# Performance work log

Measured on AMD Instinct MI355X. Metric: run time of the kernel, lower is better.

The kernel has to match this reference:

```python
import jax, jax.numpy as jnp
import numpy as np

H, W, C = 64, 64, 64
B = 64
N_HEADS = 4
CONV_FILTERS = 64
BASIS_DIM = 16


def get_spatial_basis(h, w, d):
    half_d = d // 2
    basis = np.zeros((h, w, d), dtype=np.float32)
    div = np.exp(np.arange(0, half_d, 2, dtype=np.float32) * -np.log(100.0) / half_d)
    h_grid = np.expand_dims(np.arange(0, h, dtype=np.float32), 1)
    w_grid = np.expand_dims(np.arange(0, w, dtype=np.float32), 1)
    basis[:, :, 0:half_d:2] = np.sin(h_grid * div)[:, np.newaxis, :]
    basis[:, :, 1:half_d:2] = np.cos(h_grid * div)[:, np.newaxis, :]
    basis[:, :, half_d::2] = np.sin(w_grid * div)[np.newaxis, :, :]
    basis[:, :, half_d + 1::2] = np.cos(w_grid * div)[np.newaxis, :, :]
    return basis


def setup_inputs() -> dict:
    key = jax.random.key(0)
    ks = jax.random.split(key, 8)
    feat_in = C + BASIS_DIM  # 80 input channels for 1x1 convs
    return {
        "image": jax.random.normal(ks[0], (B, H, W, C), jnp.float32),
        "state1": jax.random.normal(ks[1], (B, 512), jnp.float32),
        "state2": jax.random.normal(ks[2], (B, 512), jnp.float32),
        "extra": jax.random.normal(ks[3], (B, 256), jnp.float32),
        "Wq": jax.random.normal(ks[4], (1024, CONV_FILTERS), jnp.float32) * 0.03,
        "bq": jnp.zeros((CONV_FILTERS,), jnp.float32),
        "Wk": jax.random.normal(ks[5], (feat_in, CONV_FILTERS), jnp.float32) * 0.1,
        "bk": jnp.zeros((CONV_FILTERS,), jnp.float32),
        "Wv": jax.random.normal(ks[6], (feat_in, CONV_FILTERS), jnp.float32) * 0.1,
        "bv": jnp.zeros((CONV_FILTERS,), jnp.float32),
        "spatial_basis": jnp.asarray(get_spatial_basis(H, W, BASIS_DIM)),
    }


def reference(image, state1, state2, extra, Wq, bq, Wk, bk, Wv, bv, spatial_basis):
    b, h, w, _ = image.shape
    nh = N_HEADS
    cf = Wq.shape[1]
    dph = cf // nh  # depth per head

    # concat image with tiled spatial basis -> [B,h,w,C+basis_dim]
    sb = jnp.broadcast_to(spatial_basis[None], (b,) + spatial_basis.shape)
    feats = jnp.concatenate([image, sb], axis=-1)

    # combiner over network-state tensors, then Dense query
    state = jnp.concatenate([state1, state2], axis=-1)  # [B,1024]
    q = state @ Wq + bq                                 # [B,cf]

    # 1x1 convs == per-pixel dense projections
    keys = feats @ Wk + bk    # [B,h,w,cf]
    vals = feats @ Wv + bv    # [B,h,w,cf]

    qh = q.reshape(b, nh, dph)
    kh = keys.reshape(b, h * w, nh, dph)
    vh = vals.reshape(b, h * w, nh, dph)

    # per-head dot scores over spatial positions, softmax over positions
    scores = jnp.einsum('bnd,bpnd->bpn', qh, kh)        # [B,hw,nh]
    attn = jax.nn.softmax(scores, axis=1)
    mean_attn = attn.mean(axis=-1).reshape(b, h, w)

    # weighted sum of values over spatial positions -> [B,cf]
    pooled = jnp.einsum('bpn,bpnd->bnd', attn, vh).reshape(b, cf)

    out = jnp.concatenate([pooled, extra], axis=-1)
    return out, mean_attn
```

## Files before the change

### kernel.cpp

```cpp
#include <hip/hip_runtime.h>
#include <hip/hip_bf16.h>

#define BATCH 64
#define HW    4096
#define PT    128
#define NS    32
#define FR_ST 104
#define FT_ST 136

typedef unsigned int u32;
typedef unsigned short u16;
typedef __attribute__((ext_vector_type(8))) short bf16x8;
typedef __attribute__((ext_vector_type(4))) float f32x4;

__device__ __forceinline__ float bf2f(u16 h) { return __uint_as_float(((u32)h) << 16); }
__device__ __forceinline__ u32 f2bf(float x) {
  u32 b = __float_as_uint(x);
  return (b + 0x7fffu + ((b >> 16) & 1u)) >> 16;
}
__device__ __forceinline__ u32 pkbf(float lo, float hi) { return f2bf(lo) | (f2bf(hi) << 16); }

template<bool F32>
__device__ __forceinline__ float ld(const void* p, size_t i) {
  if (F32) return ((const float*)p)[i];
  return bf2f(((const u16*)p)[i]);
}
template<bool F32>
__device__ __forceinline__ float4 ld4(const void* p, size_t i4) {
  if (F32) return ((const float4*)p)[i4];
  uint2 u = ((const uint2*)p)[i4];
  return make_float4(bf2f(u.x & 0xffff), bf2f(u.x >> 16), bf2f(u.y & 0xffff), bf2f(u.y >> 16));
}
template<bool F32>
__device__ __forceinline__ void st(void* p, size_t i, float v) {
  if (F32) ((float*)p)[i] = v;
  else     ((__hip_bfloat16*)p)[i] = __float2bfloat16(v);
}

__device__ __forceinline__ bool detect_f32(const u16* __restrict__ image) {
  u16 h = image[(threadIdx.x & 63) * 2];
  u32 e = (h >> 7) & 0xFFu;
  unsigned long long m = __ballot(e >= 0x86u);
  return __popcll(m) >= 8;
}

template<bool F32>
__device__ void k1a_body(const void* state1, const void* state2, const void* Wq,
                         float* q_part, float* WslT, float* stt) {
  const int kb = blockIdx.x;
  const int tid = threadIdx.x;
#pragma unroll
  for (int i = 0; i < 4; ++i) {
    const int fidx = i * 256 + tid;
    const int r = fidx >> 4, c4 = fidx & 15;
    float4 v = ld4<F32>(Wq, (size_t)(kb * 64 + r) * 16 + c4);
    WslT[(c4 * 4 + 0) * 68 + r] = v.x;
    WslT[(c4 * 4 + 1) * 68 + r] = v.y;
    WslT[(c4 * 4 + 2) * 68 + r] = v.z;
    WslT[(c4 * 4 + 3) * 68 + r] = v.w;
  }
  const void* src = (kb < 8) ? state1 : state2;
  const int k0q = (kb & 7) * 16;
#pragma unroll
  for (int i = 0; i < 4; ++i) {
    const int fidx = i * 256 + tid;
    const int bb = fidx >> 4, i4 = fidx & 15;
    float4 v = ld4<F32>(src, (size_t)bb * 128 + k0q + i4);
    *(float4*)&stt[bb * 64 + i4 * 4] = v;
  }
  __syncthreads();
  const int j = tid & 63, bg = tid >> 6;
  float acc[16];
#pragma unroll
  for (int b2 = 0; b2 < 16; ++b2) acc[b2] = 0.f;
#pragma unroll
  for (int i4 = 0; i4 < 16; ++i4) {
    float4 wv = *(const float4*)&WslT[j * 68 + i4 * 4];
#pragma unroll
    for (int b2 = 0; b2 < 16; ++b2) {
      float4 sv = *(const float4*)&stt[(bg * 16 + b2) * 64 + i4 * 4];
      acc[b2] += wv.x * sv.x + wv.y * sv.y + wv.z * sv.z + wv.w * sv.w;
    }
  }
#pragma unroll
  for (int b2 = 0; b2 < 16; ++b2)
    q_part[kb * 4096 + (bg * 16 + b2) * 64 + j] = acc[b2];
}

__global__ __launch_bounds__(256) void k1a(
    const void* image, const void* state1, const void* state2, const void* Wq, float* q_part) {
  __shared__ float WslT[64 * 68];
  __shared__ float stt[64 * 64];
  if (detect_f32((const u16*)image)) k1a_body<true >(state1, state2, Wq, q_part, WslT, stt);
  else                               k1a_body<false>(state1, state2, Wq, q_part, WslT, stt);
}

template<bool F32>
__device__ void k1b_body(const float* q_part, const void* bq, const void* Wk, const void* bk,
                         u16* weffbt, float* cb, float* q) {
  const int b = blockIdx.x, tid = threadIdx.x;
  u32* wz = (u32*)(weffbt + (size_t)b * 1664);
  for (int i = tid; i < 832; i += 320) wz[i] = 0u;
  if (tid < 64) {
    float a = ld<F32>(bq, tid);
#pragma unroll
    for (int sl = 0; sl < 16; ++sl) a += q_part[sl * 4096 + b * 64 + tid];
    q[tid] = a;
  }
  __syncthreads();
  if (tid < 320) {
    const int c = tid >> 2, n = tid & 3;
    float a = 0.f;
#pragma unroll
    for (int d = 0; d < 16; ++d) a += ld<F32>(Wk, (size_t)c * 64 + n * 16 + d) * q[n * 16 + d];
    weffbt[(size_t)b * 1664 + n * 104 + c] = (u16)f2bf(a);
  }
  if (tid >= 256 && tid < 260) {
    const int n = tid - 256;
    float a = 0.f;
#pragma unroll
    for (int d = 0; d < 16; ++d) a += ld<F32>(bk, n * 16 + d) * q[n * 16 + d];
    cb[b * 4 + n] = a;
  }
}

__global__ __launch_bounds__(320) void k1b(
    const void* image, const float* q_part, const void* bq, const void* Wk, const void* bk,
    u16* weffbt, float* cb) {
  __shared__ float q[64];
  if (detect_f32((const u16*)image)) k1b_body<true >(q_part, bq, Wk, bk, weffbt, cb, q);
  else                               k1b_body<false>(q_part, bq, Wk, bk, weffbt, cb, q);
}

__global__ __launch_bounds__(256) void k2_main(
    const void* __restrict__ image, const void* __restrict__ basis,
    const float* __restrict__ cb, const u16* __restrict__ weffbt,
    u16* __restrict__ e_buf, float* __restrict__ m_blk, float* __restrict__ sum_blk,
    float* __restrict__ fpool_part) {
  __shared__ __align__(16) u16 smem[25936];
  float* redf  = (float*)(smem + 25856);
  float* red2f = (float*)(smem + 25888);
  float* bmf   = (float*)(smem + 25920);
  float* cbL   = (float*)(smem + 25928);

  const int tid = threadIdx.x;
  const int b = blockIdx.x & 63, s = blockIdx.x >> 6;
  const int bs = b * NS + s;
  const int wave = tid >> 6, lane = tid & 63;
  const int m = lane & 15, q = lane >> 4;

  if (detect_f32((const u16*)image)) {
    const float4* img4 = (const float4*)image + ((size_t)(b * HW + s * PT)) * 16;
#pragma unroll
    for (int i = 0; i < 4; ++i) {
      const int fidx = i * 256 + tid;
      const int pq = fidx >> 4, c4 = fidx & 15;
      float4 v0 = img4[(pq * 2) * 16 + c4];
      float4 v1 = img4[(pq * 2 + 1) * 16 + c4];
      *(uint2*)&smem[(pq * 2) * FR_ST + c4 * 4]     = make_uint2(pkbf(v0.x, v0.y), pkbf(v0.z, v0.w));
      *(uint2*)&smem[(pq * 2 + 1) * FR_ST + c4 * 4] = make_uint2(pkbf(v1.x, v1.y), pkbf(v1.z, v1.w));
      const float a0[4] = {v0.x, v0.y, v0.z, v0.w};
      const float a1[4] = {v1.x, v1.y, v1.z, v1.w};
#pragma unroll
      for (int k = 0; k < 4; ++k)
        *(u32*)&smem[13312 + (c4 * 4 + k) * FT_ST + pq * 2] = pkbf(a0[k], a1[k]);
    }
    const float4* bas4 = (const float4*)basis + (size_t)(s * PT) * 4;
    {
      const int pq = tid >> 2, c4 = tid & 3;
      float4 v0 = bas4[(pq * 2) * 4 + c4];
      float4 v1 = bas4[(pq * 2 + 1) * 4 + c4];
      *(uint2*)&smem[(pq * 2) * FR_ST + 64 + c4 * 4]     = make_uint2(pkbf(v0.x, v0.y), pkbf(v0.z, v0.w));
      *(uint2*)&smem[(pq * 2 + 1) * FR_ST + 64 + c4 * 4] = make_uint2(pkbf(v1.x, v1.y), pkbf(v1.z, v1.w));
      const float a0[4] = {v0.x, v0.y, v0.z, v0.w};
      const float a1[4] = {v1.x, v1.y, v1.z, v1.w};
#pragma unroll
      for (int k = 0; k < 4; ++k)
        *(u32*)&smem[13312 + (64 + c4 * 4 + k) * FT_ST + pq * 2] = pkbf(a0[k], a1[k]);
    }
  } else {
    const uint4* img4 = (const uint4*)image + ((size_t)(b * HW + s * PT)) * 4;
    {
      const int pq = tid >> 2, c8 = tid & 3;
      uint4 u0 = img4[(pq * 2) * 4 + c8];
      uint4 u1 = img4[(pq * 2 + 1) * 4 + c8];
      *(uint4*)&smem[(pq * 2) * FR_ST + c8 * 8]     = u0;
      *(uint4*)&smem[(pq * 2 + 1) * FR_ST + c8 * 8] = u1;
      const u32 w0[4] = {u0.x, u0.y, u0.z, u0.w};
      const u32 w1[4] = {u1.x, u1.y, u1.z, u1.w};
#pragma unroll
      for (int k = 0; k < 4; ++k) {
        *(u32*)&smem[13312 + (c8 * 8 + 2 * k) * FT_ST + pq * 2]     = (w0[k] & 0xffffu) | (w1[k] << 16);
        *(u32*)&smem[13312 + (c8 * 8 + 2 * k + 1) * FT_ST + pq * 2] = (w0[k] >> 16) | (w1[k] & 0xffff0000u);
      }
    }
    const uint4* bas4 = (const uint4*)basis + (size_t)(s * PT) * 2;
    if (tid < 128) {
      const int pq = tid >> 1, c8 = tid & 1;
      uint4 u0 = bas4[(pq * 2) * 2 + c8];
      uint4 u1 = bas4[(pq * 2 + 1) * 2 + c8];
      *(uint4*)&smem[(pq * 2) * FR_ST + 64 + c8 * 8]     = u0;
      *(uint4*)&smem[(pq * 2 + 1) * FR_ST + 64 + c8 * 8] = u1;
      const u32 w0[4] = {u0.x, u0.y, u0.z, u0.w};
      const u32 w1[4] = {u1.x, u1.y, u1.z, u1.w};
#pragma unroll
      for (int k = 0; k < 4; ++k) {
        *(u32*)&smem[13312 + (64 + c8 * 8 + 2 * k) * FT_ST + pq * 2]     = (w0[k] & 0xffffu) | (w1[k] << 16);
        *(u32*)&smem[13312 + (64 + c8 * 8 + 2 * k + 1) * FT_ST + pq * 2] = (w0[k] >> 16) | (w1[k] & 0xffff0000u);
      }
    }
  }
  if (tid < 128) {
    *(uint4*)&smem[tid * FR_ST + 80] = make_uint4(0, 0, 0, 0);
    *(uint4*)&smem[tid * FR_ST + 88] = make_uint4(0, 0, 0, 0);
  }
  if (tid < 208) {
    uint4 v = ((const uint4*)(weffbt + (size_t)b * 1664))[tid];
    *(uint4*)&smem[24192 + tid * 8] = v;
  }
  if (tid < 4) cbL[tid] = cb[b * 4 + tid];
  __syncthreads();

  f32x4 accS[2];
  {
    const float ci = (m < 4) ? cbL[m] : 0.f;
#pragma unroll
    for (int t = 0; t < 2; ++t) { accS[t][0] = ci; accS[t][1] = ci; accS[t][2] = ci; accS[t][3] = ci; }
#pragma unroll
    for (int t = 0; t < 2; ++t) {
      const int T = wave * 2 + t;
#pragma unroll
      for (int s3 = 0; s3 < 3; ++s3) {
        bf16x8 a = *(const bf16x8*)&smem[(T * 16 + m) * FR_ST + s3 * 32 + q * 8];
        bf16x8 bb = *(const bf16x8*)&smem[24192 + m * FR_ST + s3 * 32 + q * 8];
        accS[t] = __builtin_amdgcn_mfma_f32_16x16x32_bf16(a, bb, accS[t], 0, 0, 0);
      }
    }
  }
  {
    float mx = accS[0][0];
#pragma unroll
    for (int t = 0; t < 2; ++t)
#pragma unroll
      for (int r = 0; r < 4; ++r) mx = fmaxf(mx, accS[t][r]);
    mx = fmaxf(mx, __shfl_xor(mx, 16, 64));
    mx = fmaxf(mx, __shfl_xor(mx, 32, 64));
    if (lane < 4) redf[wave * 4 + lane] = mx;
  }
  __syncthreads();
  if (tid < 4)
    bmf[tid] = fmaxf(fmaxf(redf[tid], redf[4 + tid]), fmaxf(redf[8 + tid], redf[12 + tid]));
  for (int i = tid; i < 816; i += 256) ((u32*)smem)[272 + i] = 0u;
  __syncthreads();

  {
    const float bmv = bmf[m & 3];
    float ss = 0.f;
#pragma unroll
    for (int t = 0; t < 2; ++t) {
      const int T = wave * 2 + t;
#pragma unroll
      for (int r = 0; r < 4; ++r) {
        float e = __expf(accS[t][r] - bmv);
        u32 eb = f2bf(e);
        float er = bf2f((u16)eb);
        ss += er;
        if (m < 4) smem[m * FT_ST + T * 16 + q * 4 + r] = (u16)eb;
      }
    }
    ss += __shfl_xor(ss, 16, 64);
    ss += __shfl_xor(ss, 32, 64);
    if (lane < 4) red2f[wave * 4 + lane] = ss;
  }
  __syncthreads();
  if (tid < 4) {
    m_blk[bs * 4 + tid] = bmf[tid];
    sum_blk[bs * 4 + tid] = red2f[tid] + red2f[4 + tid] + red2f[8 + tid] + red2f[12 + tid];
  }
  {
    const int n = tid >> 6, pp = tid & 63;
    u32 v = *(const u32*)&smem[n * FT_ST + pp * 2];
    ((u32*)e_buf)[((size_t)(b * 4 + n)) * 2048 + s * 64 + pp] = v;
  }
  {
    bf16x8 ap = *(const bf16x8*)&smem[m * FT_ST + wave * 32 + q * 8];
    f32x4 accP[5];
#pragma unroll
    for (int T = 0; T < 5; ++T) { accP[T][0] = 0; accP[T][1] = 0; accP[T][2] = 0; accP[T][3] = 0; }
#pragma unroll
    for (int T = 0; T < 5; ++T) {
      bf16x8 bp = *(const bf16x8*)&smem[13312 + (T * 16 + m) * FT_ST + wave * 32 + q * 8];
      accP[T] = __builtin_amdgcn_mfma_f32_16x16x32_bf16(ap, bp, accP[T], 0, 0, 0);
    }
    if (lane < 16) {
      float* pr = (float*)(smem + 2176);
#pragma unroll
      for (int T = 0; T < 5; ++T)
#pragma unroll
        for (int r = 0; r < 4; ++r)
          pr[((wave * 5 + T) * 4 + r) * 16 + lane] = accP[T][r];
    }
  }
  __syncthreads();
  {
    const float* pr = (const float*)(smem + 2176);
    for (int t = tid; t < 320; t += 256) {
      const int n = t / 80, c = t - n * 80;
      const int tile = c >> 4, cc = c & 15;
      float a = 0.f;
#pragma unroll
      for (int w = 0; w < 4; ++w) a += pr[((w * 5 + tile) * 4 + n) * 16 + cc];
      fpool_part[(size_t)bs * 320 + t] = a;
    }
  }
}

template<bool F32>
__device__ void k34_body(const float* m_blk, const float* sum_blk, const u16* e_buf,
                         const float* fpool_part, const void* Wv, const void* bv,
                         const void* extra, void* out, float* esc, float* fp) {
  const int tid = threadIdx.x;
  const int b = blockIdx.x & 63, s16 = blockIdx.x >> 6;
  if (tid < 4) {
    float M = -3.4e38f;
#pragma unroll
    for (int sp = 0; sp < NS; ++sp) M = fmaxf(M, m_blk[(b * NS + sp) * 4 + tid]);
    float den = 0.f;
#pragma unroll
    for (int sp = 0; sp < NS; ++sp)
      den += __expf(m_blk[(b * NS + sp) * 4 + tid] - M) * sum_blk[(b * NS + sp) * 4 + tid];
    float rd = 1.0f / den;
#pragma unroll
    for (int sp = 0; sp < NS; ++sp)
      esc[sp * 4 + tid] = __expf(m_blk[(b * NS + sp) * 4 + tid] - M) * rd;
  }
  __syncthreads();
  {
    const int gpos = s16 * 256 + tid;
    const int s32 = gpos >> 7;
    float mean = 0.f;
#pragma unroll
    for (int n = 0; n < 4; ++n)
      mean += bf2f(e_buf[(size_t)(b * 4 + n) * HW + gpos]) * esc[s32 * 4 + n];
    st<F32>(out, (size_t)BATCH * 320 + (size_t)b * HW + gpos, 0.25f * mean);
  }
  if (s16 == 0) {
    for (int idx = tid; idx < 320; idx += 256) {
      const int n2 = idx / 80;
      float a = 0.f;
#pragma unroll
      for (int sp = 0; sp < NS; ++sp)
        a += esc[sp * 4 + n2] * fpool_part[(size_t)(b * NS + sp) * 320 + idx];
      fp[idx] = a;
    }
    __syncthreads();
    if (tid < 64) {
      const int n = tid >> 4;
      float dot = 0.f;
#pragma unroll
      for (int c = 0; c < 80; ++c) dot += fp[n * 80 + c] * ld<F32>(Wv, (size_t)c * 64 + tid);
      st<F32>(out, (size_t)b * 320 + tid, dot + ld<F32>(bv, tid));
    }
    st<F32>(out, (size_t)b * 320 + 64 + tid, ld<F32>(extra, (size_t)b * 256 + tid));
  }
}

__global__ __launch_bounds__(256) void k34_out(
    const void* image, const float* m_blk, const float* sum_blk, const u16* e_buf,
    const float* fpool_part, const void* Wv, const void* bv, const void* extra, void* out) {
  __shared__ float esc[NS * 4];
  __shared__ float fp[320];
  if (detect_f32((const u16*)image))
       k34_body<true >(m_blk, sum_blk, e_buf, fpool_part, Wv, bv, extra, out, esc, fp);
  else k34_body<false>(m_blk, sum_blk, e_buf, fpool_part, Wv, bv, extra, out, esc, fp);
}

extern "C" void kernel_launch(void* const* d_in, const int* in_sizes, int n_in,
                              void* d_out, int out_size, void* d_ws, size_t ws_size,
                              hipStream_t stream) {
  (void)in_sizes; (void)n_in; (void)out_size; (void)ws_size;
  const void* image  = d_in[0];
  const void* state1 = d_in[1];
  const void* state2 = d_in[2];
  const void* extra  = d_in[3];
  const void* Wq = d_in[4];
  const void* bq = d_in[5];
  const void* Wk = d_in[6];
  const void* bk = d_in[7];
  const void* Wv = d_in[8];
  const void* bv = d_in[9];
  const void* basis = d_in[10];

  float* ws         = (float*)d_ws;
  float* cb         = ws;
  float* m_blk      = ws + 256;
  float* sum_blk    = ws + 8448;
  float* q_part     = ws + 16640;
  float* fpool_part = ws + 82176;
  u16*   weffbt     = (u16*)(ws + 737536);
  u16*   e_buf      = (u16*)(ws + 790784);

  k1a<<<dim3(16), dim3(256), 0, stream>>>(image, state1, state2, Wq, q_part);
  k1b<<<dim3(BATCH), dim3(320), 0, stream>>>(image, q_part, bq, Wk, bk, weffbt, cb);
  k2_main<<<dim3(BATCH * NS), dim3(256), 0, stream>>>(image, basis, cb, weffbt,
                                                      e_buf, m_blk, sum_blk, fpool_part);
  k34_out<<<dim3(BATCH * 16), dim3(256), 0, stream>>>(image, m_blk, sum_blk, e_buf,
                                                      fpool_part, Wv, bv, extra, d_out);
}
```

Baseline: 131.5 us.

## Merge query prep kernels and load score operands directly from global memory

The two query-preparation kernels become a single per-batch kernel that computes the state·Wq product and the effective key weights in one launch, which drops one launch and the q_part round trip. In the main kernel the row-major bf16 feature copy in shared memory is removed. The score MFMA now reads its A operands straight from global image/basis, and its B weights go into registers instead of LDS. Shared memory use shrinks and launch bounds ask for 4 blocks per CU to raise occupancy, at the cost of reading the image from global memory twice per tile (once for the transposed LDS copy, once for the scores).

```diff
diff --git a/kernel.cpp b/kernel.cpp
--- a/kernel.cpp
+++ b/kernel.cpp
@@ -5,8 +5,13 @@
 #define HW    4096
 #define PT    128
 #define NS    32
-#define FR_ST 104
 #define FT_ST 136
+
+#define FT_BASE  0
+#define EST_BASE 10880
+#define PR_BASE  13056
+#define RED_BASE 15616
+#define SMEM_TOT 15680
 
 typedef unsigned int u32;
 typedef unsigned short u16;
@@ -24,12 +29,6 @@
 __device__ __forceinline__ float ld(const void* p, size_t i) {
   if (F32) return ((const float*)p)[i];
   return bf2f(((const u16*)p)[i]);
-}
-template<bool F32>
-__device__ __forceinline__ float4 ld4(const void* p, size_t i4) {
-  if (F32) return ((const float4*)p)[i4];
-  uint2 u = ((const uint2*)p)[i4];
-  return make_float4(bf2f(u.x & 0xffff), bf2f(u.x >> 16), bf2f(u.y & 0xffff), bf2f(u.y >> 16));
 }
 template<bool F32>
 __device__ __forceinline__ void st(void* p, size_t i, float v) {
@@ -45,111 +44,70 @@
 }
 
 template<bool F32>
-__device__ void k1a_body(const void* state1, const void* state2, const void* Wq,
-                         float* q_part, float* WslT, float* stt) {
-  const int kb = blockIdx.x;
-  const int tid = threadIdx.x;
-#pragma unroll
-  for (int i = 0; i < 4; ++i) {
-    const int fidx = i * 256 + tid;
-    const int r = fidx >> 4, c4 = fidx & 15;
-    float4 v = ld4<F32>(Wq, (size_t)(kb * 64 + r) * 16 + c4);
-    WslT[(c4 * 4 + 0) * 68 + r] = v.x;
-    WslT[(c4 * 4 + 1) * 68 + r] = v.y;
-    WslT[(c4 * 4 + 2) * 68 + r] = v.z;
-    WslT[(c4 * 4 + 3) * 68 + r] = v.w;
-  }
-  const void* src = (kb < 8) ? state1 : state2;
-  const int k0q = (kb & 7) * 16;
-#pragma unroll
-  for (int i = 0; i < 4; ++i) {
-    const int fidx = i * 256 + tid;
-    const int bb = fidx >> 4, i4 = fidx & 15;
-    float4 v = ld4<F32>(src, (size_t)bb * 128 + k0q + i4);
-    *(float4*)&stt[bb * 64 + i4 * 4] = v;
-  }
-  __syncthreads();
-  const int j = tid & 63, bg = tid >> 6;
-  float acc[16];
-#pragma unroll
-  for (int b2 = 0; b2 < 16; ++b2) acc[b2] = 0.f;
-#pragma unroll
-  for (int i4 = 0; i4 < 16; ++i4) {
-    float4 wv = *(const float4*)&WslT[j * 68 + i4 * 4];
-#pragma unroll
-    for (int b2 = 0; b2 < 16; ++b2) {
-      float4 sv = *(const float4*)&stt[(bg * 16 + b2) * 64 + i4 * 4];
-      acc[b2] += wv.x * sv.x + wv.y * sv.y + wv.z * sv.z + wv.w * sv.w;
-    }
-  }
-#pragma unroll
-  for (int b2 = 0; b2 < 16; ++b2)
-    q_part[kb * 4096 + (bg * 16 + b2) * 64 + j] = acc[b2];
-}
-
-__global__ __launch_bounds__(256) void k1a(
-    const void* image, const void* state1, const void* state2, const void* Wq, float* q_part) {
-  __shared__ float WslT[64 * 68];
-  __shared__ float stt[64 * 64];
-  if (detect_f32((const u16*)image)) k1a_body<true >(state1, state2, Wq, q_part, WslT, stt);
-  else                               k1a_body<false>(state1, state2, Wq, q_part, WslT, stt);
-}
-
-template<bool F32>
-__device__ void k1b_body(const float* q_part, const void* bq, const void* Wk, const void* bk,
-                         u16* weffbt, float* cb, float* q) {
+__device__ void k1_body(const void* state1, const void* state2, const void* Wq, const void* bq,
+                        const void* Wk, const void* bk, u16* weffbt, float* cb,
+                        float* stt, float* qp, float* q) {
   const int b = blockIdx.x, tid = threadIdx.x;
+  for (int i = tid; i < 512; i += 256) {
+    stt[i]       = ld<F32>(state1, (size_t)b * 512 + i);
+    stt[512 + i] = ld<F32>(state2, (size_t)b * 512 + i);
+  }
   u32* wz = (u32*)(weffbt + (size_t)b * 1664);
-  for (int i = tid; i < 832; i += 320) wz[i] = 0u;
-  if (tid < 64) {
-    float a = ld<F32>(bq, tid);
-#pragma unroll
-    for (int sl = 0; sl < 16; ++sl) a += q_part[sl * 4096 + b * 64 + tid];
-    q[tid] = a;
-  }
-  __syncthreads();
-  if (tid < 320) {
-    const int c = tid >> 2, n = tid & 3;
+  for (int i = tid; i < 832; i += 256) wz[i] = 0u;
+  __syncthreads();
+  {
+    const int j = tid & 63, g = tid >> 6, i0 = g * 256;
+    float a = 0.f;
+#pragma unroll 8
+    for (int i = 0; i < 256; ++i) a += stt[i0 + i] * ld<F32>(Wq, (size_t)(i0 + i) * 64 + j);
+    qp[g * 64 + j] = a;
+  }
+  __syncthreads();
+  if (tid < 64) q[tid] = qp[tid] + qp[64 + tid] + qp[128 + tid] + qp[192 + tid] + ld<F32>(bq, tid);
+  __syncthreads();
+  for (int t = tid; t < 320; t += 256) {
+    const int c = t >> 2, n = t & 3;
     float a = 0.f;
 #pragma unroll
     for (int d = 0; d < 16; ++d) a += ld<F32>(Wk, (size_t)c * 64 + n * 16 + d) * q[n * 16 + d];
     weffbt[(size_t)b * 1664 + n * 104 + c] = (u16)f2bf(a);
   }
-  if (tid >= 256 && tid < 260) {
-    const int n = tid - 256;
+  if (tid < 4) {
     float a = 0.f;
 #pragma unroll
-    for (int d = 0; d < 16; ++d) a += ld<F32>(bk, n * 16 + d) * q[n * 16 + d];
-    cb[b * 4 + n] = a;
-  }
-}
-
-__global__ __launch_bounds__(320) void k1b(
-    const void* image, const float* q_part, const void* bq, const void* Wk, const void* bk,
-    u16* weffbt, float* cb) {
+    for (int d = 0; d < 16; ++d) a += ld<F32>(bk, tid * 16 + d) * q[tid * 16 + d];
+    cb[b * 4 + tid] = a;
+  }
+}
+
+__global__ __launch_bounds__(256) void k1_prep(
+    const void* image, const void* state1, const void* state2, const void* Wq, const void* bq,
+    const void* Wk, const void* bk, u16* weffbt, float* cb) {
+  __shared__ float stt[1024];
+  __shared__ float qp[256];
   __shared__ float q[64];
-  if (detect_f32((const u16*)image)) k1b_body<true >(q_part, bq, Wk, bk, weffbt, cb, q);
-  else                               k1b_body<false>(q_part, bq, Wk, bk, weffbt, cb, q);
-}
-
-__global__ __launch_bounds__(256) void k2_main(
+  if (detect_f32((const u16*)image))
+       k1_body<true >(state1, state2, Wq, bq, Wk, bk, weffbt, cb, stt, qp, q);
+  else k1_body<false>(state1, state2, Wq, bq, Wk, bk, weffbt, cb, stt, qp, q);
+}
+
+__global__ __launch_bounds__(256, 4) void k2_main(
     const void* __restrict__ image, const void* __restrict__ basis,
     const float* __restrict__ cb, const u16* __restrict__ weffbt,
     u16* __restrict__ e_buf, float* __restrict__ m_blk, float* __restrict__ sum_blk,
     float* __restrict__ fpool_part) {
-  __shared__ __align__(16) u16 smem[25936];
-  float* redf  = (float*)(smem + 25856);
-  float* red2f = (float*)(smem + 25888);
-  float* bmf   = (float*)(smem + 25920);
-  float* cbL   = (float*)(smem + 25928);
+  __shared__ __align__(16) u16 smem[SMEM_TOT];
+  float* redf  = (float*)(smem + RED_BASE);
+  float* red2f = (float*)(smem + RED_BASE + 32);
 
   const int tid = threadIdx.x;
   const int b = blockIdx.x & 63, s = blockIdx.x >> 6;
   const int bs = b * NS + s;
   const int wave = tid >> 6, lane = tid & 63;
   const int m = lane & 15, q = lane >> 4;
-
-  if (detect_f32((const u16*)image)) {
+  const bool isf32 = detect_f32((const u16*)image);
+
+  if (isf32) {
     const float4* img4 = (const float4*)image + ((size_t)(b * HW + s * PT)) * 16;
 #pragma unroll
     for (int i = 0; i < 4; ++i) {
@@ -157,26 +115,20 @@
       const int pq = fidx >> 4, c4 = fidx & 15;
       float4 v0 = img4[(pq * 2) * 16 + c4];
       float4 v1 = img4[(pq * 2 + 1) * 16 + c4];
-      *(uint2*)&smem[(pq * 2) * FR_ST + c4 * 4]     = make_uint2(pkbf(v0.x, v0.y), pkbf(v0.z, v0.w));
-      *(uint2*)&smem[(pq * 2 + 1) * FR_ST + c4 * 4] = make_uint2(pkbf(v1.x, v1.y), pkbf(v1.z, v1.w));
-      const float a0[4] = {v0.x, v0.y, v0.z, v0.w};
-      const float a1[4] = {v1.x, v1.y, v1.z, v1.w};
-#pragma unroll
-      for (int k = 0; k < 4; ++k)
-        *(u32*)&smem[13312 + (c4 * 4 + k) * FT_ST + pq * 2] = pkbf(a0[k], a1[k]);
+      *(u32*)&smem[FT_BASE + (c4 * 4 + 0) * FT_ST + pq * 2] = pkbf(v0.x, v1.x);
+      *(u32*)&smem[FT_BASE + (c4 * 4 + 1) * FT_ST + pq * 2] = pkbf(v0.y, v1.y);
+      *(u32*)&smem[FT_BASE + (c4 * 4 + 2) * FT_ST + pq * 2] = pkbf(v0.z, v1.z);
+      *(u32*)&smem[FT_BASE + (c4 * 4 + 3) * FT_ST + pq * 2] = pkbf(v0.w, v1.w);
     }
     const float4* bas4 = (const float4*)basis + (size_t)(s * PT) * 4;
     {
       const int pq = tid >> 2, c4 = tid & 3;
       float4 v0 = bas4[(pq * 2) * 4 + c4];
       float4 v1 = bas4[(pq * 2 + 1) * 4 + c4];
-      *(uint2*)&smem[(pq * 2) * FR_ST + 64 + c4 * 4]     = make_uint2(pkbf(v0.x, v0.y), pkbf(v0.z, v0.w));
-      *(uint2*)&smem[(pq * 2 + 1) * FR_ST + 64 + c4 * 4] = make_uint2(pkbf(v1.x, v1.y), pkbf(v1.z, v1.w));
-      const float a0[4] = {v0.x, v0.y, v0.z, v0.w};
-      const float a1[4] = {v1.x, v1.y, v1.z, v1.w};
-#pragma unroll
-      for (int k = 0; k < 4; ++k)
-        *(u32*)&smem[13312 + (64 + c4 * 4 + k) * FT_ST + pq * 2] = pkbf(a0[k], a1[k]);
+      *(u32*)&smem[FT_BASE + (64 + c4 * 4 + 0) * FT_ST + pq * 2] = pkbf(v0.x, v1.x);
+      *(u32*)&smem[FT_BASE + (64 + c4 * 4 + 1) * FT_ST + pq * 2] = pkbf(v0.y, v1.y);
+      *(u32*)&smem[FT_BASE + (64 + c4 * 4 + 2) * FT_ST + pq * 2] = pkbf(v0.z, v1.z);
+      *(u32*)&smem[FT_BASE + (64 + c4 * 4 + 3) * FT_ST + pq * 2] = pkbf(v0.w, v1.w);
     }
   } else {
     const uint4* img4 = (const uint4*)image + ((size_t)(b * HW + s * PT)) * 4;
@@ -184,14 +136,12 @@
       const int pq = tid >> 2, c8 = tid & 3;
       uint4 u0 = img4[(pq * 2) * 4 + c8];
       uint4 u1 = img4[(pq * 2 + 1) * 4 + c8];
-      *(uint4*)&smem[(pq * 2) * FR_ST + c8 * 8]     = u0;
-      *(uint4*)&smem[(pq * 2 + 1) * FR_ST + c8 * 8] = u1;
       const u32 w0[4] = {u0.x, u0.y, u0.z, u0.w};
       const u32 w1[4] = {u1.x, u1.y, u1.z, u1.w};
 #pragma unroll
       for (int k = 0; k < 4; ++k) {
-        *(u32*)&smem[13312 + (c8 * 8 + 2 * k) * FT_ST + pq * 2]     = (w0[k] & 0xffffu) | (w1[k] << 16);
-        *(u32*)&smem[13312 + (c8 * 8 + 2 * k + 1) * FT_ST + pq * 2] = (w0[k] >> 16) | (w1[k] & 0xffff0000u);
+        *(u32*)&smem[FT_BASE + (c8 * 8 + 2 * k) * FT_ST + pq * 2]     = (w0[k] & 0xffffu) | (w1[k] << 16);
+        *(u32*)&smem[FT_BASE + (c8 * 8 + 2 * k + 1) * FT_ST + pq * 2] = (w0[k] >> 16) | (w1[k] & 0xffff0000u);
       }
     }
     const uint4* bas4 = (const uint4*)basis + (size_t)(s * PT) * 2;
@@ -199,41 +149,50 @@
       const int pq = tid >> 1, c8 = tid & 1;
       uint4 u0 = bas4[(pq * 2) * 2 + c8];
       uint4 u1 = bas4[(pq * 2 + 1) * 2 + c8];
-      *(uint4*)&smem[(pq * 2) * FR_ST + 64 + c8 * 8]     = u0;
-      *(uint4*)&smem[(pq * 2 + 1) * FR_ST + 64 + c8 * 8] = u1;
       const u32 w0[4] = {u0.x, u0.y, u0.z, u0.w};
       const u32 w1[4] = {u1.x, u1.y, u1.z, u1.w};
 #pragma unroll
       for (int k = 0; k < 4; ++k) {
-        *(u32*)&smem[13312 + (64 + c8 * 8 + 2 * k) * FT_ST + pq * 2]     = (w0[k] & 0xffffu) | (w1[k] << 16);
-        *(u32*)&smem[13312 + (64 + c8 * 8 + 2 * k + 1) * FT_ST + pq * 2] = (w0[k] >> 16) | (w1[k] & 0xffff0000u);
+        *(u32*)&smem[FT_BASE + (64 + c8 * 8 + 2 * k) * FT_ST + pq * 2]     = (w0[k] & 0xffffu) | (w1[k] << 16);
+        *(u32*)&smem[FT_BASE + (64 + c8 * 8 + 2 * k + 1) * FT_ST + pq * 2] = (w0[k] >> 16) | (w1[k] & 0xffff0000u);
       }
     }
   }
-  if (tid < 128) {
-    *(uint4*)&smem[tid * FR_ST + 80] = make_uint4(0, 0, 0, 0);
-    *(uint4*)&smem[tid * FR_ST + 88] = make_uint4(0, 0, 0, 0);
-  }
-  if (tid < 208) {
-    uint4 v = ((const uint4*)(weffbt + (size_t)b * 1664))[tid];
-    *(uint4*)&smem[24192 + tid * 8] = v;
-  }
-  if (tid < 4) cbL[tid] = cb[b * 4 + tid];
-  __syncthreads();
-
+
+  bf16x8 bfr[3];
+  {
+    const u16* wrow = weffbt + (size_t)b * 1664 + m * 104;
+#pragma unroll
+    for (int s3 = 0; s3 < 3; ++s3) bfr[s3] = *(const bf16x8*)&wrow[s3 * 32 + q * 8];
+  }
   f32x4 accS[2];
   {
-    const float ci = (m < 4) ? cbL[m] : 0.f;
+    const float ci = (m < 4) ? cb[b * 4 + m] : 0.f;
 #pragma unroll
     for (int t = 0; t < 2; ++t) { accS[t][0] = ci; accS[t][1] = ci; accS[t][2] = ci; accS[t][3] = ci; }
 #pragma unroll
     for (int t = 0; t < 2; ++t) {
-      const int T = wave * 2 + t;
+      const int p = s * PT + (wave * 2 + t) * 16 + m;
 #pragma unroll
       for (int s3 = 0; s3 < 3; ++s3) {
-        bf16x8 a = *(const bf16x8*)&smem[(T * 16 + m) * FR_ST + s3 * 32 + q * 8];
-        bf16x8 bb = *(const bf16x8*)&smem[24192 + m * FR_ST + s3 * 32 + q * 8];
-        accS[t] = __builtin_amdgcn_mfma_f32_16x16x32_bf16(a, bb, accS[t], 0, 0, 0);
+        bf16x8 a;
+        if (isf32) {
+          float4 v0, v1;
+          if (s3 < 2) {
+            const float4* ip = (const float4*)image + ((size_t)b * HW + p) * 16 + s3 * 8 + q * 2;
+            v0 = ip[0]; v1 = ip[1];
+          } else if (q < 2) {
+            const float4* bp = (const float4*)basis + (size_t)p * 4 + q * 2;
+            v0 = bp[0]; v1 = bp[1];
+          } else { v0 = make_float4(0, 0, 0, 0); v1 = v0; }
+          u32 aw[4] = {pkbf(v0.x, v0.y), pkbf(v0.z, v0.w), pkbf(v1.x, v1.y), pkbf(v1.z, v1.w)};
+          a = *(const bf16x8*)aw;
+        } else {
+          if (s3 < 2) a = *(const bf16x8*)&((const u16*)image)[((size_t)b * HW + p) * 64 + s3 * 32 + q * 8];
+          else if (q < 2) a = *(const bf16x8*)&((const u16*)basis)[(size_t)p * 16 + q * 8];
+          else { u32 z[4] = {0, 0, 0, 0}; a = *(const bf16x8*)z; }
+        }
+        accS[t] = __builtin_amdgcn_mfma_f32_16x16x32_bf16(a, bfr[s3], accS[t], 0, 0, 0);
       }
     }
   }
@@ -248,13 +207,13 @@
     if (lane < 4) redf[wave * 4 + lane] = mx;
   }
   __syncthreads();
-  if (tid < 4)
-    bmf[tid] = fmaxf(fmaxf(redf[tid], redf[4 + tid]), fmaxf(redf[8 + tid], redf[12 + tid]));
-  for (int i = tid; i < 816; i += 256) ((u32*)smem)[272 + i] = 0u;
-  __syncthreads();
-
-  {
-    const float bmv = bmf[m & 3];
+
+  float bmv;
+  {
+    const int hh = m & 3;
+    bmv = fmaxf(fmaxf(redf[hh], redf[4 + hh]), fmaxf(redf[8 + hh], redf[12 + hh]));
+  }
+  {
     float ss = 0.f;
 #pragma unroll
     for (int t = 0; t < 2; ++t) {
@@ -263,9 +222,8 @@
       for (int r = 0; r < 4; ++r) {
         float e = __expf(accS[t][r] - bmv);
         u32 eb = f2bf(e);
-        float er = bf2f((u16)eb);
-        ss += er;
-        if (m < 4) smem[m * FT_ST + T * 16 + q * 4 + r] = (u16)eb;
+        ss += bf2f((u16)eb);
+        if (m < 4) smem[EST_BASE + m * FT_ST + T * 16 + q * 4 + r] = (u16)eb;
       }
     }
     ss += __shfl_xor(ss, 16, 64);
@@ -273,27 +231,29 @@
     if (lane < 4) red2f[wave * 4 + lane] = ss;
   }
   __syncthreads();
+
   if (tid < 4) {
-    m_blk[bs * 4 + tid] = bmf[tid];
-    sum_blk[bs * 4 + tid] = red2f[tid] + red2f[4 + tid] + red2f[8 + tid] + red2f[12 + tid];
+    const int hh = tid;
+    m_blk[bs * 4 + hh] = fmaxf(fmaxf(redf[hh], redf[4 + hh]), fmaxf(redf[8 + hh], redf[12 + hh]));
+    sum_blk[bs * 4 + hh] = red2f[hh] + red2f[4 + hh] + red2f[8 + hh] + red2f[12 + hh];
   }
   {
     const int n = tid >> 6, pp = tid & 63;
-    u32 v = *(const u32*)&smem[n * FT_ST + pp * 2];
+    u32 v = *(const u32*)&smem[EST_BASE + n * FT_ST + pp * 2];
     ((u32*)e_buf)[((size_t)(b * 4 + n)) * 2048 + s * 64 + pp] = v;
   }
   {
-    bf16x8 ap = *(const bf16x8*)&smem[m * FT_ST + wave * 32 + q * 8];
+    bf16x8 ap = *(const bf16x8*)&smem[EST_BASE + m * FT_ST + wave * 32 + q * 8];
     f32x4 accP[5];
 #pragma unroll
     for (int T = 0; T < 5; ++T) { accP[T][0] = 0; accP[T][1] = 0; accP[T][2] = 0; accP[T][3] = 0; }
 #pragma unroll
     for (int T = 0; T < 5; ++T) {
-      bf16x8 bp = *(const bf16x8*)&smem[13312 + (T * 16 + m) * FT_ST + wave * 32 + q * 8];
+      bf16x8 bp = *(const bf16x8*)&smem[FT_BASE + (T * 16 + m) * FT_ST + wave * 32 + q * 8];
       accP[T] = __builtin_amdgcn_mfma_f32_16x16x32_bf16(ap, bp, accP[T], 0, 0, 0);
     }
     if (lane < 16) {
-      float* pr = (float*)(smem + 2176);
+      float* pr = (float*)(smem + PR_BASE);
 #pragma unroll
       for (int T = 0; T < 5; ++T)
 #pragma unroll
@@ -303,7 +263,7 @@
   }
   __syncthreads();
   {
-    const float* pr = (const float*)(smem + 2176);
+    const float* pr = (const float*)(smem + PR_BASE);
     for (int t = tid; t < 320; t += 256) {
       const int n = t / 80, c = t - n * 80;
       const int tile = c >> 4, cc = c & 15;
@@ -395,13 +355,11 @@
   float* cb         = ws;
   float* m_blk      = ws + 256;
   float* sum_blk    = ws + 8448;
-  float* q_part     = ws + 16640;
-  float* fpool_part = ws + 82176;
-  u16*   weffbt     = (u16*)(ws + 737536);
-  u16*   e_buf      = (u16*)(ws + 790784);
-
-  k1a<<<dim3(16), dim3(256), 0, stream>>>(image, state1, state2, Wq, q_part);
-  k1b<<<dim3(BATCH), dim3(320), 0, stream>>>(image, q_part, bq, Wk, bk, weffbt, cb);
+  float* fpool_part = ws + 16640;
+  u16*   weffbt     = (u16*)(ws + 672000);
+  u16*   e_buf      = (u16*)(ws + 725248);
+
+  k1_prep<<<dim3(BATCH), dim3(256), 0, stream>>>(image, state1, state2, Wq, bq, Wk, bk, weffbt, cb);
   k2_main<<<dim3(BATCH * NS), dim3(256), 0, stream>>>(image, basis, cb, weffbt,
                                                       e_buf, m_blk, sum_blk, fpool_part);
   k34_out<<<dim3(BATCH * 16), dim3(256), 0, stream>>>(image, m_blk, sum_blk, e_buf,
```

After: 139.5 us. 6.0% more time.
